# Performance work log

Hardware: AMD Instinct MI355X
Metric: run time of the kernel (lower is better)

Reference implementation:

```python
import jax, jax.numpy as jnp
from jax import lax
import numpy as np

B, D_IN, L, D, K, DS = 8, 16, 4096, 512, 4, 4
BLOCKS = (1, 2, 3, 4)          # block sizes, all offset 0 (max_block_size=4)
PAD_MULT = 12                  # lcm(1,2,3,4)


def setup_inputs() -> dict:
    key = jax.random.key(0)
    ks = jax.random.split(key, 5)
    return {
        "x": jax.random.normal(ks[0], (B, D_IN, L), jnp.float32),
        "conv_w": jax.random.normal(ks[1], (D, D_IN, K), jnp.float32) * 0.05,
        "conv_b": jax.random.normal(ks[2], (D,), jnp.float32) * 0.02,
        "score_w": jax.random.normal(ks[3], (D,), jnp.float32) * 0.02,
        "score_b": jax.random.normal(ks[4], (1,), jnp.float32) * 0.02,
    }


def reference(x, conv_w, conv_b, score_w, score_b):
    # pos_conv: Conv1d(padding='same', k=4). Torch 'same' with even kernel pads
    # left=(k-1)//2=1, right=2.
    h = lax.conv_general_dilated(x, conv_w, (1,), [(1, 2)],
                                 dimension_numbers=('NCH', 'OIH', 'NCH'))
    h = jnp.transpose(h, (0, 2, 1)) + conv_b            # [B, L, D]

    Np = -(-L // PAD_MULT) * PAD_MULT                   # pad seq to multiple of 12
    h = jnp.pad(h, ((0, 0), (0, Np - L), (0, 0)))       # [B, Np, D]

    # per-block-size mean pooling, then broadcast back to char resolution
    reprs = []
    for m in BLOCKS:
        r = h.reshape(B, Np // m, m, D).mean(axis=2)    # [B, Np/m, D]
        reprs.append(jnp.repeat(r, m, axis=1))          # [B, Np, D]
    br = jnp.stack(reprs, axis=2)                       # [B, Np, nb, D]

    # score each block representation, softmax over block sizes
    scores = jnp.einsum('bnmd,d->bnm', br, score_w) + score_b[0]
    scores = jax.nn.softmax(scores, axis=2)             # [B, Np, nb]

    # consensus attention across positions over the nb-dim score vectors
    sim = jnp.einsum('bim,bjm->bij', scores, scores)    # [B, Np, Np]
    attn = jax.nn.softmax(sim, axis=-1)
    scores = jnp.einsum('bij,bjm->bim', attn, scores)   # [B, Np, nb]

    # weighted sum of block reprs
    xo = jnp.einsum('bnmd,bnm->bnd', br, scores)        # [B, Np, D]

    mlen = -(-L // DS) * DS                              # 4096 (== L here)
    char_x = xo[:, :mlen]
    xd = char_x.reshape(B, mlen // DS, DS, D).mean(axis=2)  # [B, L/DS, D]
    return char_x[:, :L], xd
```

## Files before the change

kernel.cpp:

```cpp
#include <hip/hip_runtime.h>
#include <hip/hip_bf16.h>

#define B_ 8
#define DIN 16
#define L_ 4096
#define D_ 512
#define NP 4104
#define NG 342
#define JSP 32
#define JCH 129
#define SPAN 48
#define NSPAN 86

__device__ __forceinline__ unsigned short f2bf(float f) {
  unsigned int u = __float_as_uint(f);
  unsigned int r = (u + 0x7fffu + ((u >> 16) & 1u)) >> 16;
  return (unsigned short)r;
}
__device__ __forceinline__ float bf2f(unsigned int u) {
  return __uint_as_float(u << 16);
}

__device__ __constant__ float D5[6] = {0.9999544f, 1.0005163f, 0.4975827f,
                                       0.1726558f, 0.0334570f, 0.0140872f};
__device__ __constant__ float FACT[6] = {1.f, 1.f, 2.f, 6.f, 24.f, 120.f};

__global__ __launch_bounds__(256) void k_uprep(
    const float* __restrict__ cw, const float* __restrict__ cb,
    const float* __restrict__ sw, float* __restrict__ us) {
  __shared__ float red[4][64];
  __shared__ float red2[64];
  int t = threadIdx.x;
  int p = t & 63, chunk = t >> 6;
  float s = 0.f;
  for (int d = chunk * 128; d < chunk * 128 + 128; ++d)
    s = fmaf(sw[d], cw[((size_t)d << 6) + p], s);
  red[chunk][p] = s;
  if (t < 64) {
    float pc = 0.f;
    for (int j = 0; j < 8; ++j) pc = fmaf(sw[t + 64 * j], cb[t + 64 * j], pc);
    red2[t] = pc;
  }
  __syncthreads();
  if (t < 64) us[t] = red[0][t] + red[1][t] + red[2][t] + red[3][t];
  if (t == 0) {
    float c0 = 0.f;
    for (int j = 0; j < 64; ++j) c0 += red2[j];
    us[64] = c0;
  }
}

__global__ __launch_bounds__(192) void k_scores(
    const float* __restrict__ x, const float* __restrict__ us,
    const float* __restrict__ sb, unsigned short* __restrict__ s0) {
  __shared__ float xs[DIN * 195];
  __shared__ float ul[65];
  __shared__ float tb[192];
  int bid = blockIdx.x;
  int b = bid / 22, blk = bid - b * 22;
  int base0 = blk * 192;
  int t = threadIdx.x;
  const float* xb = x + (size_t)b * DIN * L_;
  for (int q = t; q < DIN * 195; q += 192) {
    int i = q / 195, c = q - i * 195;
    int nx = base0 - 1 + c;
    xs[q] = (nx >= 0 && nx < L_) ? xb[i * L_ + nx] : 0.f;
  }
  if (t < 65) ul[t] = us[t];
  __syncthreads();
  int n = base0 + t;
  float tv = 0.f;
  if (n < L_) {
    tv = ul[64];
    for (int i = 0; i < DIN; ++i) {
#pragma unroll
      for (int k = 0; k < 4; ++k)
        tv = fmaf(xs[i * 195 + t + k], ul[(i << 2) + k], tv);
    }
  }
  tb[t] = tv;
  __syncthreads();
  if (n < NP) {
    float t1 = tb[t];
    int e2 = t & ~1;
    float t2 = 0.5f * (tb[e2] + tb[e2 + 1]);
    int e3 = (t / 3) * 3;
    float t3 = (1.f / 3.f) * (tb[e3] + tb[e3 + 1] + tb[e3 + 2]);
    int e4 = t & ~3;
    float t4 = 0.25f * (tb[e4] + tb[e4 + 1] + tb[e4 + 2] + tb[e4 + 3]);
    float sbv = sb[0];
    float c0s = t1 + sbv, c1s = t2 + sbv, c2s = t3 + sbv, c3s = t4 + sbv;
    float mx = fmaxf(fmaxf(c0s, c1s), fmaxf(c2s, c3s));
    float e0 = __expf(c0s - mx), e1 = __expf(c1s - mx);
    float e2f = __expf(c2s - mx), e3f = __expf(c3s - mx);
    float inv = 1.f / (e0 + e1 + e2f + e3f);
    ushort4 ov;
    ov.x = f2bf(e0 * inv); ov.y = f2bf(e1 * inv);
    ov.z = f2bf(e2f * inv); ov.w = f2bf(e3f * inv);
    *reinterpret_cast<ushort4*>(&s0[(((size_t)b * NP) + n) << 2]) = ov;
  }
}

__global__ __launch_bounds__(256) void k_moment(
    const unsigned short* __restrict__ s0, float* __restrict__ Mpart) {
  __shared__ float sv[JCH][4];
  __shared__ float ls[JCH][4];
  __shared__ float mp[4][128][5];
  int bid = blockIdx.x;
  int js = bid & 31;
  int b = bid >> 5;
  int t = threadIdx.x;
  int lane = t & 63, wv = t >> 6;
  int jlo = js * JCH;
  int cnt = NP - jlo; if (cnt > JCH) cnt = JCH;

  const ushort4* sp = reinterpret_cast<const ushort4*>(s0) + (size_t)b * NP + jlo;
  for (int r = t; r < cnt; r += 256) {
    ushort4 u = sp[r];
    float v0 = bf2f(u.x), v1 = bf2f(u.y), v2 = bf2f(u.z), v3 = bf2f(u.w);
    sv[r][0] = v0; sv[r][1] = v1; sv[r][2] = v2; sv[r][3] = v3;
    ls[r][0] = __log2f(v0); ls[r][1] = __log2f(v1);
    ls[r][2] = __log2f(v2); ls[r][3] = __log2f(v3);
  }
  int f1 = lane, f2 = lane + 64;
  float e1a = 0.f, e1b = 0.f, e1c = 0.f, e1d = 0.f;
  float e2a = 0.f, e2b = 0.f, e2c = 0.f, e2d = 0.f;
  {
    int f = 0;
    for (int a = 0; a <= 5; ++a)
      for (int b2 = 0; b2 <= 5 - a; ++b2)
        for (int c = 0; c <= 5 - a - b2; ++c)
          for (int d2 = 0; d2 <= 5 - a - b2 - c; ++d2) {
            if (f == f1) { e1a = a; e1b = b2; e1c = c; e1d = d2; }
            if (f == f2) { e2a = a; e2b = b2; e2c = c; e2d = d2; }
            ++f;
          }
  }
  __syncthreads();
  float acc1[5] = {0.f, 0.f, 0.f, 0.f, 0.f};
  float acc2[5] = {0.f, 0.f, 0.f, 0.f, 0.f};
  for (int jj = wv; jj < cnt; jj += 4) {
    float4 lv = *reinterpret_cast<float4*>(&ls[jj][0]);
    float4 vv = *reinterpret_cast<float4*>(&sv[jj][0]);
    float t1 = e1a * lv.x;
    t1 = fmaf(e1b, lv.y, t1);
    t1 = fmaf(e1c, lv.z, t1);
    t1 = fmaf(e1d, lv.w, t1);
    float t2 = e2a * lv.x;
    t2 = fmaf(e2b, lv.y, t2);
    t2 = fmaf(e2c, lv.z, t2);
    t2 = fmaf(e2d, lv.w, t2);
    float m1 = exp2f(t1);
    float m2 = exp2f(t2);
    acc1[0] = fmaf(m1, vv.x, acc1[0]);
    acc1[1] = fmaf(m1, vv.y, acc1[1]);
    acc1[2] = fmaf(m1, vv.z, acc1[2]);
    acc1[3] = fmaf(m1, vv.w, acc1[3]);
    acc1[4] += m1;
    acc2[0] = fmaf(m2, vv.x, acc2[0]);
    acc2[1] = fmaf(m2, vv.y, acc2[1]);
    acc2[2] = fmaf(m2, vv.z, acc2[2]);
    acc2[3] = fmaf(m2, vv.w, acc2[3]);
    acc2[4] += m2;
  }
#pragma unroll
  for (int c = 0; c < 5; ++c) {
    mp[wv][lane][c] = acc1[c];
    mp[wv][lane + 64][c] = acc2[c];
  }
  __syncthreads();
  if (t < 630) {
    int f = t / 5, c = t - f * 5;
    float s = mp[0][f][c] + mp[1][f][c] + mp[2][f][c] + mp[3][f][c];
    Mpart[((size_t)(b * 32 + js)) * 640 + t] = s;
  }
}

__global__ __launch_bounds__(640) void k_mred(
    const float* __restrict__ Mpart, float* __restrict__ Mfin) {
  int b = blockIdx.x;
  int t = threadIdx.x;
  if (t >= 630) return;
  int f = t / 5, c = t - f * 5;
  float s = 0.f;
  for (int js = 0; js < JSP; ++js)
    s += Mpart[((size_t)(b * 32 + js)) * 640 + t];
  int fa = 0, fb = 0, fc = 0, fd = 0;
  {
    int ff = 0;
    for (int a = 0; a <= 5; ++a)
      for (int b2 = 0; b2 <= 5 - a; ++b2)
        for (int cc = 0; cc <= 5 - a - b2; ++cc)
          for (int d2 = 0; d2 <= 5 - a - b2 - cc; ++d2) {
            if (ff == f) { fa = a; fb = b2; fc = cc; fd = d2; }
            ++ff;
          }
  }
  int k = fa + fb + fc + fd;
  float w = D5[k] * FACT[k] / (FACT[fa] * FACT[fb] * FACT[fc] * FACT[fd]);
  Mfin[((size_t)b * 128 + f) * 8 + c] = w * s;
}

__global__ __launch_bounds__(256) void k_apply(
    const unsigned short* __restrict__ s0, const float* __restrict__ Mfin,
    float* __restrict__ s2) {
  __shared__ float M[128 * 8];
  int bid = blockIdx.x;
  int b = bid / 17, ch = bid - b * 17;
  int t = threadIdx.x;
  const float4* Mb = reinterpret_cast<const float4*>(Mfin + (size_t)b * 128 * 8);
  if (t < 252) *reinterpret_cast<float4*>(&M[t * 4]) = Mb[t];
  __syncthreads();
  int i = ch * 256 + t;
  if (i >= NP) return;
  ushort4 u = reinterpret_cast<const ushort4*>(s0)[(size_t)b * NP + i];
  float s_0 = bf2f(u.x), s_1 = bf2f(u.y), s_2 = bf2f(u.z), s_3 = bf2f(u.w);
  float a0 = 0.f, a1 = 0.f, a2 = 0.f, a3 = 0.f, az = 0.f;
  int f = 0;
  float pa = 1.f;
#pragma unroll
  for (int a = 0; a <= 5; ++a) {
    float pb = pa;
#pragma unroll
    for (int b2 = 0; b2 <= 5 - a; ++b2) {
      float pc = pb;
#pragma unroll
      for (int c = 0; c <= 5 - a - b2; ++c) {
        float run = pc;
#pragma unroll
        for (int d2 = 0; d2 <= 5 - a - b2 - c; ++d2) {
          const float* mf = &M[f * 8];
          float4 m4 = *reinterpret_cast<const float4*>(mf);
          a0 = fmaf(run, m4.x, a0);
          a1 = fmaf(run, m4.y, a1);
          a2 = fmaf(run, m4.z, a2);
          a3 = fmaf(run, m4.w, a3);
          az = fmaf(run, mf[4], az);
          run *= s_3;
          ++f;
        }
        pc *= s_2;
      }
      pb *= s_1;
    }
    pa *= s_0;
  }
  float inv = 1.f / az;
  reinterpret_cast<float4*>(s2)[(size_t)b * NP + i] =
      make_float4(a0 * inv, a1 * inv, a2 * inv, a3 * inv);
}

__global__ __launch_bounds__(256) void k_fused(
    const float* __restrict__ x, const float* __restrict__ cw,
    const float* __restrict__ cb, const float* __restrict__ s2,
    float* __restrict__ out) {
  __shared__ float ws_w[64 * 132];
  __shared__ float ws_x[DIN * 52];
  __shared__ float ss[4][12][4];
  int bid = blockIdx.x;
  int dtile = bid & 3;
  int span = (bid >> 2) % NSPAN;
  int b = bid / (4 * NSPAN);
  int n0 = span * SPAN;
  int d0 = dtile * 128;
  int g0 = n0 / 12;
  int tid = threadIdx.x;

  for (int q = tid; q < 128 * 16; q += 256) {
    int dd = q >> 4, qq = (q & 15) << 2;
    float4 wv = *reinterpret_cast<const float4*>(cw + ((size_t)(d0 + dd) << 6) + qq);
    *reinterpret_cast<float4*>(&ws_w[(dd >> 1) * 132 + (dd & 1) * 64 + qq]) = wv;
  }
  const float* xb = x + (size_t)b * DIN * L_;
  for (int q = tid; q < DIN * 52; q += 256) {
    int i = q / 52, c = q - i * 52;
    int nx = n0 - 1 + c;
    ws_x[q] = (c < 51 && nx >= 0 && nx < L_) ? xb[i * L_ + nx] : 0.f;
  }
  if (tid < 192) {
    int gg = tid / 48, r = tid - gg * 48;
    int g = g0 + gg;
    ((float*)ss)[tid] = (g < NG) ? s2[((size_t)b * NP + g * 12) * 4 + r] : 0.f;
  }
  __syncthreads();

  int dp = tid & 63;
  int seg = tid >> 6;
  int g = g0 + seg;
  float acc0[12], acc1[12];
#pragma unroll
  for (int j = 0; j < 12; ++j) { acc0[j] = 0.f; acc1[j] = 0.f; }

  for (int i = 0; i < DIN; ++i) {
    const float* wp = &ws_w[dp * 132 + (i << 2)];
    float w00 = wp[0], w01 = wp[1], w02 = wp[2], w03 = wp[3];
    float w10 = wp[64], w11 = wp[65], w12 = wp[66], w13 = wp[67];
    const float* xp = &ws_x[i * 52 + seg * 12];
    float xr[16];
#pragma unroll
    for (int m = 0; m < 16; ++m) xr[m] = xp[m];
#pragma unroll
    for (int j = 0; j < 12; ++j) {
      float a0 = acc0[j], a1 = acc1[j];
      a0 = fmaf(w00, xr[j], a0);
      a0 = fmaf(w01, xr[j + 1], a0);
      a0 = fmaf(w02, xr[j + 2], a0);
      a0 = fmaf(w03, xr[j + 3], a0);
      a1 = fmaf(w10, xr[j], a1);
      a1 = fmaf(w11, xr[j + 1], a1);
      a1 = fmaf(w12, xr[j + 2], a1);
      a1 = fmaf(w13, xr[j + 3], a1);
      acc0[j] = a0; acc1[j] = a1;
    }
  }
  if (g >= NG) return;

  int d = d0 + (dp << 1);
  float cb0 = cb[d], cb1 = cb[d + 1];
  int base = g * 12;
  float hv0[12], hv1[12];
#pragma unroll
  for (int j = 0; j < 12; ++j) {
    int n = base + j;
    if (n < L_) { hv0[j] = acc0[j] + cb0; hv1[j] = acc1[j] + cb1; }
    else { hv0[j] = 0.f; hv1[j] = 0.f; }
  }
  float P20[6], P21[6], P30[4], P31[4], P40[3], P41[3];
#pragma unroll
  for (int q = 0; q < 6; ++q) {
    P20[q] = 0.5f * (hv0[2 * q] + hv0[2 * q + 1]);
    P21[q] = 0.5f * (hv1[2 * q] + hv1[2 * q + 1]);
  }
#pragma unroll
  for (int q = 0; q < 4; ++q) {
    P30[q] = (1.f / 3.f) * (hv0[3 * q] + hv0[3 * q + 1] + hv0[3 * q + 2]);
    P31[q] = (1.f / 3.f) * (hv1[3 * q] + hv1[3 * q + 1] + hv1[3 * q + 2]);
  }
#pragma unroll
  for (int q = 0; q < 3; ++q) {
    P40[q] = 0.25f * (hv0[4 * q] + hv0[4 * q + 1] + hv0[4 * q + 2] + hv0[4 * q + 3]);
    P41[q] = 0.25f * (hv1[4 * q] + hv1[4 * q + 1] + hv1[4 * q + 2] + hv1[4 * q + 3]);
  }
  float* outc = out;
  float* outd = out + (size_t)B_ * L_ * D_;
  float xq0[3] = {0.f, 0.f, 0.f}, xq1[3] = {0.f, 0.f, 0.f};
#pragma unroll
  for (int j = 0; j < 12; ++j) {
    float w0 = ss[seg][j][0], w1 = ss[seg][j][1];
    float w2 = ss[seg][j][2], w3 = ss[seg][j][3];
    float v0 = w0 * hv0[j] + w1 * P20[j >> 1] + w2 * P30[j / 3] + w3 * P40[j >> 2];
    float v1 = w0 * hv1[j] + w1 * P21[j >> 1] + w2 * P31[j / 3] + w3 * P41[j >> 2];
    int n = base + j;
    if (n < L_) {
      float2 o; o.x = v0; o.y = v1;
      *reinterpret_cast<float2*>(&outc[((size_t)b * L_ + n) * D_ + d]) = o;
    }
    xq0[j >> 2] += v0; xq1[j >> 2] += v1;
  }
#pragma unroll
  for (int q = 0; q < 3; ++q) {
    int r = 3 * g + q;
    if (r < 1024) {
      float2 o; o.x = 0.25f * xq0[q]; o.y = 0.25f * xq1[q];
      *reinterpret_cast<float2*>(&outd[((size_t)b * 1024 + r) * D_ + d]) = o;
    }
  }
}

extern "C" void kernel_launch(void* const* d_in, const int* in_sizes, int n_in,
                              void* d_out, int out_size, void* d_ws, size_t ws_size,
                              hipStream_t stream) {
  const float* x = (const float*)d_in[0];
  const float* cw = (const float*)d_in[1];
  const float* cb = (const float*)d_in[2];
  const float* sw = (const float*)d_in[3];
  const float* sb = (const float*)d_in[4];
  float* out = (float*)d_out;
  char* ws = (char*)d_ws;
  size_t off = 0;
  unsigned short* s0 = (unsigned short*)(ws + off);
  off += 262656;
  float* s2 = (float*)(ws + off);
  off += 525312;
  float* Mpart = (float*)(ws + off);
  off += 655360;
  float* Mfin = (float*)(ws + off);
  off += 32768;
  float* us = (float*)(ws + off);

  k_uprep<<<1, 256, 0, stream>>>(cw, cb, sw, us);
  k_scores<<<8 * 22, 192, 0, stream>>>(x, us, sb, s0);
  k_moment<<<B_ * JSP, 256, 0, stream>>>(s0, Mpart);
  k_mred<<<B_, 640, 0, stream>>>(Mpart, Mfin);
  k_apply<<<B_ * 17, 256, 0, stream>>>(s0, Mfin, s2);
  k_fused<<<B_ * NSPAN * 4, 256, 0, stream>>>(x, cw, cb, s2, out);
}
```

Measured before the change: 76.83 us.

## Fold prep and moment-reduce kernels into neighbors, vectorize LDS loads in conv

```diff
diff --git a/kernel.cpp b/kernel.cpp
--- a/kernel.cpp
+++ b/kernel.cpp
@@ -25,35 +25,13 @@
                                        0.1726558f, 0.0334570f, 0.0140872f};
 __device__ __constant__ float FACT[6] = {1.f, 1.f, 2.f, 6.f, 24.f, 120.f};
 
-__global__ __launch_bounds__(256) void k_uprep(
-    const float* __restrict__ cw, const float* __restrict__ cb,
-    const float* __restrict__ sw, float* __restrict__ us) {
-  __shared__ float red[4][64];
-  __shared__ float red2[64];
-  int t = threadIdx.x;
-  int p = t & 63, chunk = t >> 6;
-  float s = 0.f;
-  for (int d = chunk * 128; d < chunk * 128 + 128; ++d)
-    s = fmaf(sw[d], cw[((size_t)d << 6) + p], s);
-  red[chunk][p] = s;
-  if (t < 64) {
-    float pc = 0.f;
-    for (int j = 0; j < 8; ++j) pc = fmaf(sw[t + 64 * j], cb[t + 64 * j], pc);
-    red2[t] = pc;
-  }
-  __syncthreads();
-  if (t < 64) us[t] = red[0][t] + red[1][t] + red[2][t] + red[3][t];
-  if (t == 0) {
-    float c0 = 0.f;
-    for (int j = 0; j < 64; ++j) c0 += red2[j];
-    us[64] = c0;
-  }
-}
-
 __global__ __launch_bounds__(192) void k_scores(
-    const float* __restrict__ x, const float* __restrict__ us,
+    const float* __restrict__ x, const float* __restrict__ cw,
+    const float* __restrict__ cb, const float* __restrict__ sw,
     const float* __restrict__ sb, unsigned short* __restrict__ s0) {
   __shared__ float xs[DIN * 195];
+  __shared__ float red[3][64];
+  __shared__ float redc[3];
   __shared__ float ul[65];
   __shared__ float tb[192];
   int bid = blockIdx.x;
@@ -66,7 +44,22 @@
     int nx = base0 - 1 + c;
     xs[q] = (nx >= 0 && nx < L_) ? xb[i * L_ + nx] : 0.f;
   }
-  if (t < 65) ul[t] = us[t];
+  {
+    int e = t & 63, grp = t >> 6;
+    int dlo = grp * 171, dhi = (grp == 2) ? 512 : (dlo + 171);
+    float s = 0.f;
+    for (int d = dlo; d < dhi; ++d)
+      s = fmaf(sw[d], cw[((size_t)d << 6) + e], s);
+    red[grp][e] = s;
+    if (e == 0) {
+      float pc = 0.f;
+      for (int d = dlo; d < dhi; ++d) pc = fmaf(sw[d], cb[d], pc);
+      redc[grp] = pc;
+    }
+  }
+  __syncthreads();
+  if (t < 64) ul[t] = red[0][t] + red[1][t] + red[2][t];
+  if (t == 64) ul[64] = redc[0] + redc[1] + redc[2];
   __syncthreads();
   int n = base0 + t;
   float tv = 0.f;
@@ -172,44 +165,38 @@
   if (t < 630) {
     int f = t / 5, c = t - f * 5;
     float s = mp[0][f][c] + mp[1][f][c] + mp[2][f][c] + mp[3][f][c];
-    Mpart[((size_t)(b * 32 + js)) * 640 + t] = s;
-  }
-}
-
-__global__ __launch_bounds__(640) void k_mred(
-    const float* __restrict__ Mpart, float* __restrict__ Mfin) {
-  int b = blockIdx.x;
-  int t = threadIdx.x;
-  if (t >= 630) return;
-  int f = t / 5, c = t - f * 5;
-  float s = 0.f;
-  for (int js = 0; js < JSP; ++js)
-    s += Mpart[((size_t)(b * 32 + js)) * 640 + t];
-  int fa = 0, fb = 0, fc = 0, fd = 0;
-  {
-    int ff = 0;
-    for (int a = 0; a <= 5; ++a)
-      for (int b2 = 0; b2 <= 5 - a; ++b2)
-        for (int cc = 0; cc <= 5 - a - b2; ++cc)
-          for (int d2 = 0; d2 <= 5 - a - b2 - cc; ++d2) {
-            if (ff == f) { fa = a; fb = b2; fc = cc; fd = d2; }
-            ++ff;
-          }
-  }
-  int k = fa + fb + fc + fd;
-  float w = D5[k] * FACT[k] / (FACT[fa] * FACT[fb] * FACT[fc] * FACT[fd]);
-  Mfin[((size_t)b * 128 + f) * 8 + c] = w * s;
+    int fa = 0, fb = 0, fc = 0, fd = 0;
+    {
+      int ff = 0;
+      for (int a = 0; a <= 5; ++a)
+        for (int b2 = 0; b2 <= 5 - a; ++b2)
+          for (int cc = 0; cc <= 5 - a - b2; ++cc)
+            for (int d2 = 0; d2 <= 5 - a - b2 - cc; ++d2) {
+              if (ff == f) { fa = a; fb = b2; fc = cc; fd = d2; }
+              ++ff;
+            }
+    }
+    int k = fa + fb + fc + fd;
+    float w = D5[k] * FACT[k] / (FACT[fa] * FACT[fb] * FACT[fc] * FACT[fd]);
+    Mpart[((size_t)(b * 32 + js)) * 640 + t] = w * s;
+  }
 }
 
 __global__ __launch_bounds__(256) void k_apply(
-    const unsigned short* __restrict__ s0, const float* __restrict__ Mfin,
+    const unsigned short* __restrict__ s0, const float* __restrict__ Mpart,
     float* __restrict__ s2) {
   __shared__ float M[128 * 8];
   int bid = blockIdx.x;
   int b = bid / 17, ch = bid - b * 17;
   int t = threadIdx.x;
-  const float4* Mb = reinterpret_cast<const float4*>(Mfin + (size_t)b * 128 * 8);
-  if (t < 252) *reinterpret_cast<float4*>(&M[t * 4]) = Mb[t];
+  for (int e = t; e < 630; e += 256) {
+    float s = 0.f;
+#pragma unroll 4
+    for (int js = 0; js < JSP; ++js)
+      s += Mpart[((size_t)(b * 32 + js)) * 640 + e];
+    int f = e / 5, c = e - f * 5;
+    M[f * 8 + c] = s;
+  }
   __syncthreads();
   int i = ch * 256 + t;
   if (i >= NP) return;
@@ -250,7 +237,7 @@
       make_float4(a0 * inv, a1 * inv, a2 * inv, a3 * inv);
 }
 
-__global__ __launch_bounds__(256) void k_fused(
+__global__ __launch_bounds__(256, 4) void k_fused(
     const float* __restrict__ x, const float* __restrict__ cw,
     const float* __restrict__ cb, const float* __restrict__ s2,
     float* __restrict__ out) {
@@ -293,23 +280,26 @@
 
   for (int i = 0; i < DIN; ++i) {
     const float* wp = &ws_w[dp * 132 + (i << 2)];
-    float w00 = wp[0], w01 = wp[1], w02 = wp[2], w03 = wp[3];
-    float w10 = wp[64], w11 = wp[65], w12 = wp[66], w13 = wp[67];
+    float4 wv0 = *reinterpret_cast<const float4*>(wp);
+    float4 wv1 = *reinterpret_cast<const float4*>(wp + 64);
     const float* xp = &ws_x[i * 52 + seg * 12];
-    float xr[16];
-#pragma unroll
-    for (int m = 0; m < 16; ++m) xr[m] = xp[m];
+    float4 xv0 = *reinterpret_cast<const float4*>(xp);
+    float4 xv1 = *reinterpret_cast<const float4*>(xp + 4);
+    float4 xv2 = *reinterpret_cast<const float4*>(xp + 8);
+    float4 xv3 = *reinterpret_cast<const float4*>(xp + 12);
+    float xr[16] = {xv0.x, xv0.y, xv0.z, xv0.w, xv1.x, xv1.y, xv1.z, xv1.w,
+                    xv2.x, xv2.y, xv2.z, xv2.w, xv3.x, xv3.y, xv3.z, xv3.w};
 #pragma unroll
     for (int j = 0; j < 12; ++j) {
       float a0 = acc0[j], a1 = acc1[j];
-      a0 = fmaf(w00, xr[j], a0);
-      a0 = fmaf(w01, xr[j + 1], a0);
-      a0 = fmaf(w02, xr[j + 2], a0);
-      a0 = fmaf(w03, xr[j + 3], a0);
-      a1 = fmaf(w10, xr[j], a1);
-      a1 = fmaf(w11, xr[j + 1], a1);
-      a1 = fmaf(w12, xr[j + 2], a1);
-      a1 = fmaf(w13, xr[j + 3], a1);
+      a0 = fmaf(wv0.x, xr[j], a0);
+      a0 = fmaf(wv0.y, xr[j + 1], a0);
+      a0 = fmaf(wv0.z, xr[j + 2], a0);
+      a0 = fmaf(wv0.w, xr[j + 3], a0);
+      a1 = fmaf(wv1.x, xr[j], a1);
+      a1 = fmaf(wv1.y, xr[j + 1], a1);
+      a1 = fmaf(wv1.z, xr[j + 2], a1);
+      a1 = fmaf(wv1.w, xr[j + 3], a1);
       acc0[j] = a0; acc1[j] = a1;
     }
   }
@@ -384,14 +374,9 @@
   off += 525312;
   float* Mpart = (float*)(ws + off);
   off += 655360;
-  float* Mfin = (float*)(ws + off);
-  off += 32768;
-  float* us = (float*)(ws + off);
-
-  k_uprep<<<1, 256, 0, stream>>>(cw, cb, sw, us);
-  k_scores<<<8 * 22, 192, 0, stream>>>(x, us, sb, s0);
+
+  k_scores<<<8 * 22, 192, 0, stream>>>(x, cw, cb, sw, sb, s0);
   k_moment<<<B_ * JSP, 256, 0, stream>>>(s0, Mpart);
-  k_mred<<<B_, 640, 0, stream>>>(Mpart, Mfin);
-  k_apply<<<B_ * 17, 256, 0, stream>>>(s0, Mfin, s2);
+  k_apply<<<B_ * 17, 256, 0, stream>>>(s0, Mpart, s2);
   k_fused<<<B_ * NSPAN * 4, 256, 0, stream>>>(x, cw, cb, s2, out);
 }
```

Result: slower. 126.5 us (+64.6%).
